# Kernel optimization log

Hardware: AMD Instinct MI355X
Metric: run time of the kernel (lower is better)

The kernel has to match this reference:

```python
import jax, jax.numpy as jnp
import numpy as np

UNITS = 1024
IN_DIM = 1024
BATCH = 4096


def setup_inputs() -> dict:
    key = jax.random.key(0)
    ks = jax.random.split(key, 11)
    C = UNITS + IN_DIM  # concat dim
    glorot = lambda k, shp: jax.random.uniform(k, shp, jnp.float32, -1.0, 1.0) * np.sqrt(6.0 / (shp[0] + shp[1]))
    return {
        "inputs": jax.random.normal(ks[0], (BATCH, IN_DIM), jnp.float32),
        "hidden_state": jax.random.normal(ks[1], (BATCH, UNITS), jnp.float32),
        "cell_state": jax.random.normal(ks[2], (BATCH, UNITS), jnp.float32),
        "W_f": glorot(ks[3], (C, UNITS)), "b_f": jnp.ones((UNITS,), jnp.float32),  # forget bias init = ones
        "W_i": glorot(ks[4], (C, UNITS)), "b_i": jnp.zeros((UNITS,), jnp.float32),
        "W_c": glorot(ks[5], (C, UNITS)), "b_c": jnp.zeros((UNITS,), jnp.float32),
        "W_o": glorot(ks[6], (C, UNITS)), "b_o": jnp.zeros((UNITS,), jnp.float32),
    }


def reference(inputs, hidden_state, cell_state, W_f, b_f, W_i, b_i, W_c, b_c, W_o, b_o):
    # concat order matches original: (hidden_state, inputs)
    x = jnp.concatenate((hidden_state, inputs), axis=1)  # [B, U+D]
    f = jax.nn.sigmoid(x @ W_f + b_f)
    i = jax.nn.sigmoid(x @ W_i + b_i)
    c_cand = jnp.tanh(x @ W_c + b_c)
    new_cell = f * cell_state + i * c_cand
    o = jax.nn.sigmoid(x @ W_o + b_o)
    new_hidden = o * jnp.tanh(new_cell)
    return (new_hidden, new_cell)
```

## Files before the change

kernel.cpp:

```cpp
#include <hip/hip_runtime.h>
#include <hip/hip_bf16.h>

#define BATCH  4096
#define UNITS  1024
#define CDIM   2048
#define NDIM   4096

typedef __attribute__((ext_vector_type(8))) short bf16x8;
typedef __attribute__((ext_vector_type(4))) short bf16x4;
typedef __attribute__((ext_vector_type(4))) float f32x4;

__device__ __forceinline__ void gload_lds16(const void* g, void* l) {
    __builtin_amdgcn_global_load_lds(
        (const __attribute__((address_space(1))) unsigned int*)g,
        (__attribute__((address_space(3))) unsigned int*)l, 16, 0, 0);
}

__device__ __forceinline__ float sigm(float x) { return 1.f / (1.f + __expf(-x)); }
__device__ __forceinline__ float tanh_fast(float x) { return 2.f / (1.f + __expf(-2.f * x)) - 1.f; }

__device__ __forceinline__ short f2bf(float f) {
    __hip_bfloat16 h = __float2bfloat16(f);
    return *reinterpret_cast<short*>(&h);
}

__global__ __launch_bounds__(256) void prep(
        const float* __restrict__ h, const float* __restrict__ in,
        const float* __restrict__ Wf, const float* __restrict__ Wi,
        const float* __restrict__ Wc, const float* __restrict__ Wo,
        __hip_bfloat16* __restrict__ x, __hip_bfloat16* __restrict__ Wt) {
    __shared__ float lds[64 * 65];
    int b = blockIdx.x, tid = threadIdx.x;
    if (b < 4096) {
        int t   = b * 256 + tid;
        int row = t >> 8;
        int c8  = (t & 255) << 3;
        const float* src = (c8 < UNITS) ? (h + (size_t)row * UNITS + c8)
                                        : (in + (size_t)row * UNITS + (c8 - UNITS));
        float4 v0 = ((const float4*)src)[0];
        float4 v1 = ((const float4*)src)[1];
        bf16x8 o;
        o[0] = f2bf(v0.x); o[1] = f2bf(v0.y); o[2] = f2bf(v0.z); o[3] = f2bf(v0.w);
        o[4] = f2bf(v1.x); o[5] = f2bf(v1.y); o[6] = f2bf(v1.z); o[7] = f2bf(v1.w);
        *(bf16x8*)(x + (size_t)row * CDIM + c8) = o;
    } else {
        int idx = b - 4096;
        int g = idx >> 9, kt = (idx >> 4) & 31, ut = idx & 15;
        const float* W = (g == 0) ? Wf : (g == 1) ? Wi : (g == 2) ? Wc : Wo;
        int k0 = kt * 64, u0 = ut * 64;
        int r16 = tid & 15, hi = tid >> 4;
#pragma unroll
        for (int it = 0; it < 4; ++it) {
            int kl = it * 16 + hi;
            float4 v = *(const float4*)&W[(size_t)(k0 + kl) * UNITS + u0 + r16 * 4];
            float* d = &lds[kl * 65 + r16 * 4];
            d[0] = v.x; d[1] = v.y; d[2] = v.z; d[3] = v.w;
        }
        __syncthreads();
#pragma unroll
        for (int it = 0; it < 4; ++it) {
            int ul = it * 16 + hi;
            int u  = u0 + ul;
            int n  = ((u >> 5) << 7) + (((u >> 4) & 1) << 6) + (g << 4) + (u & 15);
            bf16x4 o;
#pragma unroll
            for (int j = 0; j < 4; ++j) o[j] = f2bf(lds[(r16 * 4 + j) * 65 + ul]);
            *(bf16x4*)(Wt + (size_t)n * CDIM + k0 + r16 * 4) = o;
        }
    }
}

__global__ __launch_bounds__(256, 2) void gemm_lstm(
    const __hip_bfloat16* __restrict__ A,
    const __hip_bfloat16* __restrict__ Bt,
    const float* __restrict__ b_f, const float* __restrict__ b_i,
    const float* __restrict__ b_c, const float* __restrict__ b_o,
    const float* __restrict__ cell,
    float* __restrict__ out)
{
    __shared__ alignas(16) short As[3][128 * 32];
    __shared__ alignas(16) short Bs[3][256 * 32];
    const int K = CDIM;
    const int NT = K / 32;

    int bid = blockIdx.x;
    int nb  = (bid & 7) * 2 + ((bid >> 3) & 1);
    int mb  = bid >> 4;
    int m0  = mb * 128, n0 = nb * 256;

    int tid  = threadIdx.x;
    int w    = tid >> 6, lane = tid & 63;
    int quad = lane >> 4, r16 = lane & 15;
    int wn   = w * 64;

    f32x4 acc[8][4];
#pragma unroll
    for (int i = 0; i < 8; ++i)
#pragma unroll
        for (int j = 0; j < 4; ++j) acc[i][j] = (f32x4){0.f, 0.f, 0.f, 0.f};

    const short* Ag = (const short*)A  + (size_t)m0 * K;
    const short* Bg = (const short*)Bt + (size_t)n0 * K;

    auto stage = [&](short* Al, short* Bl, int kt) {
        int k0 = kt * 32;
#pragma unroll
        for (int q = 0; q < 2; ++q) {
            int s = q * 256 + tid;
            int row = s >> 2, c = (s & 3) ^ (row & 3);
            gload_lds16(Ag + (size_t)row * K + k0 + c * 8, Al + (q * 256 + wn) * 8);
        }
#pragma unroll
        for (int q = 0; q < 4; ++q) {
            int s = q * 256 + tid;
            int n = s >> 2, c = (s & 3) ^ (n & 3);
            gload_lds16(Bg + (size_t)n * K + k0 + c * 8, Bl + (q * 256 + wn) * 8);
        }
    };

    short *a0 = &As[0][0], *a1 = &As[1][0], *a2 = &As[2][0];
    short *b0 = &Bs[0][0], *b1 = &Bs[1][0], *b2 = &Bs[2][0];
    stage(a0, b0, 0);
    stage(a1, b1, 1);

    for (int t = 0; t < NT; ++t) {
        if (t < NT - 1) asm volatile("s_waitcnt vmcnt(6)" ::: "memory");
        else            asm volatile("s_waitcnt vmcnt(0)" ::: "memory");
        __builtin_amdgcn_s_barrier();
        if (t + 2 < NT) stage(a2, b2, t + 2);

        int kc = (quad ^ (r16 & 3)) * 8;
        bf16x8 af[8], bf[4];
#pragma unroll
        for (int i = 0; i < 8; ++i)
            af[i] = *(const bf16x8*)&a0[(i * 16 + r16) * 32 + kc];
#pragma unroll
        for (int j = 0; j < 4; ++j)
            bf[j] = *(const bf16x8*)&b0[(wn + j * 16 + r16) * 32 + kc];

        __builtin_amdgcn_s_setprio(1);
#pragma unroll
        for (int i = 0; i < 8; ++i)
#pragma unroll
            for (int j = 0; j < 4; ++j)
                acc[i][j] = __builtin_amdgcn_mfma_f32_16x16x32_bf16(af[i], bf[j], acc[i][j], 0, 0, 0);
        __builtin_amdgcn_s_setprio(0);

        short* ta = a0; a0 = a1; a1 = a2; a2 = ta;
        short* tb = b0; b0 = b1; b1 = b2; b2 = tb;
    }

    int u = nb * 64 + (w >> 1) * 32 + (w & 1) * 16 + r16;
    float bfv = b_f[u], biv = b_i[u], bcv = b_c[u], bov = b_o[u];
    float* out_h = out;
    float* out_c = out + (size_t)BATCH * UNITS;
#pragma unroll
    for (int i = 0; i < 8; ++i) {
#pragma unroll
        for (int rr = 0; rr < 4; ++rr) {
            int m = m0 + i * 16 + quad * 4 + rr;
            float fg = sigm(acc[i][0][rr] + bfv);
            float ig = sigm(acc[i][1][rr] + biv);
            float cc = tanh_fast(acc[i][2][rr] + bcv);
            float og = sigm(acc[i][3][rr] + bov);
            float cold = cell[(size_t)m * UNITS + u];
            float cn = fg * cold + ig * cc;
            out_h[(size_t)m * UNITS + u] = og * tanh_fast(cn);
            out_c[(size_t)m * UNITS + u] = cn;
        }
    }
}

extern "C" void kernel_launch(void* const* d_in, const int* in_sizes, int n_in,
                              void* d_out, int out_size, void* d_ws, size_t ws_size,
                              hipStream_t stream) {
    const float* inputs = (const float*)d_in[0];
    const float* hidden = (const float*)d_in[1];
    const float* cell   = (const float*)d_in[2];
    const float* Wf = (const float*)d_in[3];
    const float* bf_ = (const float*)d_in[4];
    const float* Wi = (const float*)d_in[5];
    const float* bi_ = (const float*)d_in[6];
    const float* Wc = (const float*)d_in[7];
    const float* bc_ = (const float*)d_in[8];
    const float* Wo = (const float*)d_in[9];
    const float* bo_ = (const float*)d_in[10];
    float* out = (float*)d_out;

    char* ws = (char*)d_ws;
    __hip_bfloat16* x  = (__hip_bfloat16*)ws;
    __hip_bfloat16* Wt = (__hip_bfloat16*)(ws + (16u << 20));

    prep<<<dim3(6144), dim3(256), 0, stream>>>(hidden, inputs, Wf, Wi, Wc, Wo, x, Wt);
    gemm_lstm<<<dim3(512), dim3(256), 0, stream>>>(
        x, Wt, bf_, bi_, bc_, bo_, cell, out);
}
```

Measured before the change: 211.8 us.

## Enlarge GEMM tile to 256x256 with 8 waves and phased LDS ping-pong

Measured after the change: 198.1 us. 6.5% less time.

```diff
diff --git a/kernel.cpp b/kernel.cpp
--- a/kernel.cpp
+++ b/kernel.cpp
@@ -70,7 +70,7 @@
     }
 }
 
-__global__ __launch_bounds__(256, 2) void gemm_lstm(
+__global__ __launch_bounds__(512, 2) void gemm_lstm(
     const __hip_bfloat16* __restrict__ A,
     const __hip_bfloat16* __restrict__ Bt,
     const float* __restrict__ b_f, const float* __restrict__ b_i,
@@ -78,20 +78,18 @@
     const float* __restrict__ cell,
     float* __restrict__ out)
 {
-    __shared__ alignas(16) short As[3][128 * 32];
-    __shared__ alignas(16) short Bs[3][256 * 32];
+    extern __shared__ short smem[];
     const int K = CDIM;
-    const int NT = K / 32;
 
     int bid = blockIdx.x;
     int nb  = (bid & 7) * 2 + ((bid >> 3) & 1);
     int mb  = bid >> 4;
-    int m0  = mb * 128, n0 = nb * 256;
+    int m0  = mb * 256, n0 = nb * 256;
 
     int tid  = threadIdx.x;
     int w    = tid >> 6, lane = tid & 63;
+    int wm   = w >> 2, wn2 = w & 3;
     int quad = lane >> 4, r16 = lane & 15;
-    int wn   = w * 64;
 
     f32x4 acc[8][4];
 #pragma unroll
@@ -99,74 +97,111 @@
 #pragma unroll
         for (int j = 0; j < 4; ++j) acc[i][j] = (f32x4){0.f, 0.f, 0.f, 0.f};
 
-    const short* Ag = (const short*)A  + (size_t)m0 * K;
-    const short* Bg = (const short*)Bt + (size_t)n0 * K;
-
-    auto stage = [&](short* Al, short* Bl, int kt) {
-        int k0 = kt * 32;
-#pragma unroll
-        for (int q = 0; q < 2; ++q) {
-            int s = q * 256 + tid;
-            int row = s >> 2, c = (s & 3) ^ (row & 3);
-            gload_lds16(Ag + (size_t)row * K + k0 + c * 8, Al + (q * 256 + wn) * 8);
-        }
-#pragma unroll
-        for (int q = 0; q < 4; ++q) {
-            int s = q * 256 + tid;
-            int n = s >> 2, c = (s & 3) ^ (n & 3);
-            gload_lds16(Bg + (size_t)n * K + k0 + c * 8, Bl + (q * 256 + wn) * 8);
-        }
-    };
-
-    short *a0 = &As[0][0], *a1 = &As[1][0], *a2 = &As[2][0];
-    short *b0 = &Bs[0][0], *b1 = &Bs[1][0], *b2 = &Bs[2][0];
-    stage(a0, b0, 0);
-    stage(a1, b1, 1);
-
-    for (int t = 0; t < NT; ++t) {
-        if (t < NT - 1) asm volatile("s_waitcnt vmcnt(6)" ::: "memory");
-        else            asm volatile("s_waitcnt vmcnt(0)" ::: "memory");
-        __builtin_amdgcn_s_barrier();
-        if (t + 2 < NT) stage(a2, b2, t + 2);
-
-        int kc = (quad ^ (r16 & 3)) * 8;
-        bf16x8 af[8], bf[4];
-#pragma unroll
-        for (int i = 0; i < 8; ++i)
-            af[i] = *(const bf16x8*)&a0[(i * 16 + r16) * 32 + kc];
-#pragma unroll
-        for (int j = 0; j < 4; ++j)
-            bf[j] = *(const bf16x8*)&b0[(wn + j * 16 + r16) * 32 + kc];
-
-        __builtin_amdgcn_s_setprio(1);
-#pragma unroll
-        for (int i = 0; i < 8; ++i)
-#pragma unroll
-            for (int j = 0; j < 4; ++j)
-                acc[i][j] = __builtin_amdgcn_mfma_f32_16x16x32_bf16(af[i], bf[j], acc[i][j], 0, 0, 0);
-        __builtin_amdgcn_s_setprio(0);
-
-        short* ta = a0; a0 = a1; a1 = a2; a2 = ta;
-        short* tb = b0; b0 = b1; b1 = b2; b2 = tb;
-    }
-
-    int u = nb * 64 + (w >> 1) * 32 + (w & 1) * 16 + r16;
-    float bfv = b_f[u], biv = b_i[u], bcv = b_c[u], bov = b_o[u];
+    const short* Ag0 = (const short*)A  + (size_t)(m0)       * K;
+    const short* Ag1 = (const short*)A  + (size_t)(m0 + 128) * K;
+    const short* Bg0 = (const short*)Bt + (size_t)(n0)       * K;
+    const short* Bg1 = (const short*)Bt + (size_t)(n0 + 128) * K;
+
+    short* lds = smem;
+    const short* Ard0 = lds + wm * 8192;
+    const short* Ard1 = lds + 16384 + wm * 8192;
+    const short* Brd0 = lds + 32768 + (wn2 >> 1) * 8192 + (wn2 & 1) * 4096;
+    const short* Brd1 = lds + 49152 + (wn2 >> 1) * 8192 + (wn2 & 1) * 4096;
+
+    bf16x8 bfr[4];
+
+#define STG(SRC, DSTOFF, KT)                                                   \
+    { _Pragma("unroll")                                                        \
+      for (int q_ = 0; q_ < 2; ++q_) {                                         \
+          int s_ = q_ * 512 + tid;                                             \
+          int row_ = s_ >> 3, cg_ = (s_ & 7) ^ (row_ & 7);                     \
+          gload_lds16(SRC + (size_t)row_ * K + (KT) * 64 + cg_ * 8,            \
+                      lds + (DSTOFF) + s_ * 8);                                \
+      } }
+
+#define PHASE(ARD, BRD, KS, IH, STAGE_CODE, WAIT_CODE)                         \
+    {                                                                          \
+        int kc_ = ((quad + (KS) * 4) ^ (r16 & 7)) * 8;                         \
+        bf16x8 af0 = *(const bf16x8*)&(ARD)[(((IH)*4+0)*16 + r16) * 64 + kc_]; \
+        bf16x8 af1 = *(const bf16x8*)&(ARD)[(((IH)*4+1)*16 + r16) * 64 + kc_]; \
+        bf16x8 af2 = *(const bf16x8*)&(ARD)[(((IH)*4+2)*16 + r16) * 64 + kc_]; \
+        bf16x8 af3 = *(const bf16x8*)&(ARD)[(((IH)*4+3)*16 + r16) * 64 + kc_]; \
+        if ((IH) == 0) {                                                       \
+            bfr[0] = *(const bf16x8*)&(BRD)[(0*16 + r16) * 64 + kc_];          \
+            bfr[1] = *(const bf16x8*)&(BRD)[(1*16 + r16) * 64 + kc_];          \
+            bfr[2] = *(const bf16x8*)&(BRD)[(2*16 + r16) * 64 + kc_];          \
+            bfr[3] = *(const bf16x8*)&(BRD)[(3*16 + r16) * 64 + kc_];          \
+        }                                                                      \
+        STAGE_CODE;                                                            \
+        asm volatile("s_barrier" ::: "memory");                                \
+        __builtin_amdgcn_s_setprio(1);                                         \
+        _Pragma("unroll")                                                      \
+        for (int j_ = 0; j_ < 4; ++j_) {                                       \
+            acc[(IH)*4+0][j_] = __builtin_amdgcn_mfma_f32_16x16x32_bf16(af0, bfr[j_], acc[(IH)*4+0][j_], 0, 0, 0); \
+            acc[(IH)*4+1][j_] = __builtin_amdgcn_mfma_f32_16x16x32_bf16(af1, bfr[j_], acc[(IH)*4+1][j_], 0, 0, 0); \
+            acc[(IH)*4+2][j_] = __builtin_amdgcn_mfma_f32_16x16x32_bf16(af2, bfr[j_], acc[(IH)*4+2][j_], 0, 0, 0); \
+            acc[(IH)*4+3][j_] = __builtin_amdgcn_mfma_f32_16x16x32_bf16(af3, bfr[j_], acc[(IH)*4+3][j_], 0, 0, 0); \
+        }                                                                      \
+        __builtin_amdgcn_s_setprio(0);                                         \
+        WAIT_CODE;                                                             \
+        asm volatile("s_barrier" ::: "memory");                                \
+    }
+
+#define VM2 asm volatile("s_waitcnt vmcnt(2)" ::: "memory")
+#define VM0 asm volatile("s_waitcnt vmcnt(0)" ::: "memory")
+#define NOPX ((void)0)
+
+    STG(Ag0, 0,     0)
+    STG(Ag1, 8192,  0)
+    STG(Bg0, 32768, 0)
+    STG(Bg1, 40960, 0)
+    STG(Bg0, 49152, 1)
+    VM2;
+    asm volatile("s_barrier" ::: "memory");
+
+    for (int u = 0; u < 15; ++u) {
+        int t1 = 2 * u + 1, t2 = 2 * u + 2, t3 = 2 * u + 3;
+        PHASE(Ard0, Brd0, 0, 0, STG(Ag0, 16384, t1), NOPX)
+        PHASE(Ard0, Brd0, 0, 1, STG(Ag1, 24576, t1), NOPX)
+        PHASE(Ard0, Brd0, 1, 0, STG(Bg1, 57344, t1), NOPX)
+        PHASE(Ard0, Brd0, 1, 1, STG(Bg0, 32768, t2), VM2)
+        PHASE(Ard1, Brd1, 0, 0, STG(Bg1, 40960, t2), NOPX)
+        PHASE(Ard1, Brd1, 0, 1, STG(Ag0, 0,     t2), NOPX)
+        PHASE(Ard1, Brd1, 1, 0, STG(Ag1, 8192,  t2), NOPX)
+        PHASE(Ard1, Brd1, 1, 1, STG(Bg0, 49152, t3), VM2)
+    }
+    PHASE(Ard0, Brd0, 0, 0, STG(Ag0, 16384, 31), NOPX)
+    PHASE(Ard0, Brd0, 0, 1, STG(Ag1, 24576, 31), NOPX)
+    PHASE(Ard0, Brd0, 1, 0, STG(Bg1, 57344, 31), NOPX)
+    PHASE(Ard0, Brd0, 1, 1, NOPX, VM0)
+    PHASE(Ard1, Brd1, 0, 0, NOPX, NOPX)
+    PHASE(Ard1, Brd1, 0, 1, NOPX, NOPX)
+    PHASE(Ard1, Brd1, 1, 0, NOPX, NOPX)
+    PHASE(Ard1, Brd1, 1, 1, NOPX, NOPX)
+
+#undef PHASE
+#undef STG
+#undef VM2
+#undef VM0
+#undef NOPX
+
+    int uo = nb * 64 + (wn2 >> 1) * 32 + (wn2 & 1) * 16 + r16;
+    float bfv = b_f[uo], biv = b_i[uo], bcv = b_c[uo], bov = b_o[uo];
     float* out_h = out;
     float* out_c = out + (size_t)BATCH * UNITS;
 #pragma unroll
     for (int i = 0; i < 8; ++i) {
 #pragma unroll
         for (int rr = 0; rr < 4; ++rr) {
-            int m = m0 + i * 16 + quad * 4 + rr;
+            int m = m0 + wm * 128 + i * 16 + quad * 4 + rr;
             float fg = sigm(acc[i][0][rr] + bfv);
             float ig = sigm(acc[i][1][rr] + biv);
             float cc = tanh_fast(acc[i][2][rr] + bcv);
             float og = sigm(acc[i][3][rr] + bov);
-            float cold = cell[(size_t)m * UNITS + u];
+            float cold = cell[(size_t)m * UNITS + uo];
             float cn = fg * cold + ig * cc;
-            out_h[(size_t)m * UNITS + u] = og * tanh_fast(cn);
-            out_c[(size_t)m * UNITS + u] = cn;
+            out_h[(size_t)m * UNITS + uo] = og * tanh_fast(cn);
+            out_c[(size_t)m * UNITS + uo] = cn;
         }
     }
 }
@@ -191,7 +226,14 @@
     __hip_bfloat16* x  = (__hip_bfloat16*)ws;
     __hip_bfloat16* Wt = (__hip_bfloat16*)(ws + (16u << 20));
 
+    static bool attr_set = false;
+    if (!attr_set) {
+        hipFuncSetAttribute(reinterpret_cast<const void*>(gemm_lstm),
+                            hipFuncAttributeMaxDynamicSharedMemorySize, 131072);
+        attr_set = true;
+    }
+
     prep<<<dim3(6144), dim3(256), 0, stream>>>(hidden, inputs, Wf, Wi, Wc, Wo, x, Wt);
-    gemm_lstm<<<dim3(512), dim3(256), 0, stream>>>(
+    gemm_lstm<<<dim3(256), dim3(512), 131072, stream>>>(
         x, Wt, bf_, bi_, bc_, bo_, cell, out);
 }
```
